# Optimization experiments

Hardware: AMD Instinct MI355X
Metric: run time of the kernel (lower is better)

Reference implementation:

```python
import jax, jax.numpy as jnp
import numpy as np

B, S, H = 1, 2048, 1024
NH, KVH, HD = 16, 4, 64
E, TOPK, F = 8, 2, 2048
EPS = 1e-5
THETA = 10000.0


def setup_inputs() -> dict:
    key = jax.random.key(0)
    ks = jax.random.split(key, 12)
    s = 0.02
    return {
        "hidden_states": jax.random.normal(ks[0], (B, S, H), jnp.float32),
        "position_ids": jnp.arange(S, dtype=jnp.int64).reshape(1, S),
        "ln1_w": jnp.ones((H,), jnp.float32),
        "ln2_w": jnp.ones((H,), jnp.float32),
        "wq": jax.random.normal(ks[1], (NH * HD, H), jnp.float32) * s,
        "wk": jax.random.normal(ks[2], (KVH * HD, H), jnp.float32) * s,
        "wv": jax.random.normal(ks[3], (KVH * HD, H), jnp.float32) * s,
        "wo": jax.random.normal(ks[4], (H, NH * HD), jnp.float32) * s,
        "gate_w": jax.random.normal(ks[5], (E, H), jnp.float32) * s,
        "w1": jax.random.normal(ks[6], (E, F, H), jnp.float32) * s,
        "w2": jax.random.normal(ks[7], (E, H, F), jnp.float32) * s,
        "w3": jax.random.normal(ks[8], (E, F, H), jnp.float32) * s,
    }


def rmsnorm(x, w, eps=EPS):
    xf = x.astype(jnp.float32)
    v = jnp.mean(xf * xf, axis=-1, keepdims=True)
    return (xf * jax.lax.rsqrt(v + eps)).astype(x.dtype) * w


def rotate_half(x):
    x1, x2 = jnp.split(x, 2, axis=-1)
    return jnp.concatenate([-x2, x1], axis=-1)


def attention(x, position_ids, wq, wk, wv, wo):
    q = (x @ wq.T).reshape(B, S, NH, HD).transpose(0, 2, 1, 3)   # [B,NH,S,HD]
    k = (x @ wk.T).reshape(B, S, KVH, HD).transpose(0, 2, 1, 3)  # [B,KVH,S,HD]
    v = (x @ wv.T).reshape(B, S, KVH, HD).transpose(0, 2, 1, 3)
    inv_freq = 1.0 / (THETA ** (jnp.arange(0, HD, 2, dtype=jnp.float32) / HD))
    ang = position_ids.astype(jnp.float32)[:, :, None] * inv_freq  # [B,S,HD/2]
    emb = jnp.concatenate([ang, ang], axis=-1)                     # [B,S,HD]
    cos = jnp.cos(emb)[:, None]                                    # [B,1,S,HD]
    sin = jnp.sin(emb)[:, None]
    q = q * cos + rotate_half(q) * sin
    k = k * cos + rotate_half(k) * sin
    rep = NH // KVH
    k = jnp.repeat(k, rep, axis=1)
    v = jnp.repeat(v, rep, axis=1)
    scores = jnp.einsum("bhqd,bhkd->bhqk", q, k) / np.sqrt(HD).astype(np.float32)
    causal = jnp.tril(jnp.ones((S, S), bool))
    scores = jnp.where(causal, scores, jnp.finfo(scores.dtype).min)
    attn = jax.nn.softmax(scores, axis=-1)
    ctx = jnp.einsum("bhqk,bhkd->bhqd", attn, v)
    ctx = ctx.transpose(0, 2, 1, 3).reshape(B, S, NH * HD)
    return ctx @ wo.T


def moe(x, gate_w, w1, w2, w3):
    xt = x.reshape(-1, H)                                  # [T,H]
    router_logits = xt @ gate_w.T                          # [T,E]
    probs = jax.nn.softmax(router_logits.astype(jnp.float32), axis=-1)
    topw, topi = jax.lax.top_k(probs, TOPK)                # [T,K]
    topw = topw / jnp.sum(topw, axis=-1, keepdims=True)
    topw = topw.astype(x.dtype)
    # combine weights per expert: [T,E]
    cw = jnp.sum(topw[..., None] * jax.nn.one_hot(topi, E, dtype=x.dtype), axis=1)
    h1 = jnp.einsum("th,efh->etf", xt, w1)
    h3 = jnp.einsum("th,efh->etf", xt, w3)
    g = jax.nn.silu(h1) * h3                               # [E,T,F]
    y = jnp.einsum("etf,ehf->eth", g, w2)                  # [E,T,H]
    out = jnp.einsum("eth,te->th", y, cw)
    return out.reshape(B, S, H), router_logits


def reference(hidden_states, position_ids, ln1_w, ln2_w, wq, wk, wv, wo,
              gate_w, w1, w2, w3):
    residual = hidden_states
    h = rmsnorm(hidden_states, ln1_w)
    h = attention(h, position_ids, wq, wk, wv, wo)
    h = residual + h
    residual = h
    h = rmsnorm(h, ln2_w)
    h, router_logits = moe(h, gate_w, w1, w2, w3)
    h = residual + h
    return h, router_logits
```

## Files before the change

### kernel.cpp

```cpp
#include <hip/hip_runtime.h>
#include <hip/hip_bf16.h>
#include <cstdint>

typedef unsigned short u16;
typedef __attribute__((ext_vector_type(8))) short bh8;
typedef __attribute__((ext_vector_type(4))) short sh4;
typedef __attribute__((ext_vector_type(4))) float fx4;

#define NTOK 2048
#define HDIM 1024
#define NE 8
#define FDIM 2048

#define VMCNT(n) asm volatile("s_waitcnt vmcnt(" #n ")" ::: "memory")
#define LGKM0()  asm volatile("s_waitcnt lgkmcnt(0)" ::: "memory")
#define SBAR()   __builtin_amdgcn_s_barrier()
#define SCB()    __builtin_amdgcn_sched_barrier(0)

__device__ __forceinline__ u16 f2bf(float f) {
    __hip_bfloat16 h = __float2bfloat16(f);
    return __builtin_bit_cast(u16, h);
}

__device__ __forceinline__ void gll16(const void* g, void* l) {
    __builtin_amdgcn_global_load_lds(
        (const __attribute__((address_space(1))) void*)g,
        (__attribute__((address_space(3))) void*)l, 16, 0, 0);
}

#define N8_WQ 131072
#define N8_WK 32768
#define N8_WV 32768
#define N8_WO 131072
#define N8_W  2097152
#define B0q 0
#define B1k (B0q + N8_WQ)
#define B2v (B1k + N8_WK)
#define B3o (B2v + N8_WV)
#define B4a (B3o + N8_WO)
#define B5b (B4a + N8_W)
#define B6c (B5b + N8_W)
#define N8TOT (B6c + N8_W)

__global__ __launch_bounds__(256)
void convert_all_k(const float* __restrict__ wq, const float* __restrict__ wk,
                   const float* __restrict__ wv, const float* __restrict__ wo,
                   const float* __restrict__ w1, const float* __restrict__ w2,
                   const float* __restrict__ w3, u16* __restrict__ arena) {
    int i = blockIdx.x * 256 + threadIdx.x;
    const int stride = gridDim.x * 256;
    for (; i < N8TOT; i += stride) {
        const float* src;
        int base;
        if (i < B1k)      { src = wq; base = B0q; }
        else if (i < B2v) { src = wk; base = B1k; }
        else if (i < B3o) { src = wv; base = B2v; }
        else if (i < B4a) { src = wo; base = B3o; }
        else if (i < B5b) { src = w1; base = B4a; }
        else if (i < B6c) { src = w2; base = B5b; }
        else              { src = w3; base = B6c; }
        const size_t li = (size_t)(i - base) * 8;
        const fx4 a = *(const fx4*)&src[li];
        const fx4 b = *(const fx4*)&src[li + 4];
        bh8 o;
        #pragma unroll
        for (int j = 0; j < 4; ++j) {
            o[j]     = (short)f2bf(a[j]);
            o[j + 4] = (short)f2bf(b[j]);
        }
        *(bh8*)&arena[(size_t)i * 8] = o;
    }
}

__global__ __launch_bounds__(256)
void rope_table_k(float* __restrict__ cosT, float* __restrict__ sinT) {
    int idx = blockIdx.x * 256 + threadIdx.x;
    int t = idx >> 5, i = idx & 31;
    float freq = powf(10000.0f, -(float)i * (1.0f / 32.0f));
    float ang = (float)t * freq;
    float s, c;
    sincosf(ang, &s, &c);
    cosT[idx] = c;
    sinT[idx] = s;
}

__global__ __launch_bounds__(256)
void rmsnorm_k(const float* __restrict__ X, const float* __restrict__ W, u16* __restrict__ O) {
    const int t = blockIdx.x;
    const int tid = threadIdx.x;
    const fx4 v = *(const fx4*)&X[(size_t)t * HDIM + tid * 4];
    float ss = v[0]*v[0] + v[1]*v[1] + v[2]*v[2] + v[3]*v[3];
    #pragma unroll
    for (int o = 1; o < 64; o <<= 1) ss += __shfl_xor(ss, o);
    __shared__ float red[4];
    if ((tid & 63) == 0) red[tid >> 6] = ss;
    __syncthreads();
    const float inv = rsqrtf((red[0] + red[1] + red[2] + red[3]) * (1.0f / HDIM) + 1e-5f);
    const fx4 w = *(const fx4*)&W[tid * 4];
    sh4 o4;
    #pragma unroll
    for (int i = 0; i < 4; ++i) o4[i] = (short)f2bf(v[i] * inv * w[i]);
    *(sh4*)&O[(size_t)t * HDIM + tid * 4] = o4;
}

__global__ __launch_bounds__(256)
void rmsnorm2_router_k(const float* __restrict__ X, const float* __restrict__ W,
                       const float* __restrict__ GW, u16* __restrict__ O,
                       float* __restrict__ LOGI) {
    const int t = blockIdx.x;
    const int tid = threadIdx.x;
    const fx4 v = *(const fx4*)&X[(size_t)t * HDIM + tid * 4];
    float ss = v[0]*v[0] + v[1]*v[1] + v[2]*v[2] + v[3]*v[3];
    #pragma unroll
    for (int o = 1; o < 64; o <<= 1) ss += __shfl_xor(ss, o);
    __shared__ float red[4];
    if ((tid & 63) == 0) red[tid >> 6] = ss;
    __syncthreads();
    const float inv = rsqrtf((red[0] + red[1] + red[2] + red[3]) * (1.0f / HDIM) + 1e-5f);
    const fx4 w = *(const fx4*)&W[tid * 4];
    fx4 xn;
    #pragma unroll
    for (int i = 0; i < 4; ++i) xn[i] = v[i] * inv * w[i];
    sh4 o4;
    #pragma unroll
    for (int i = 0; i < 4; ++i) o4[i] = (short)f2bf(xn[i]);
    *(sh4*)&O[(size_t)t * HDIM + tid * 4] = o4;

    float part[NE];
    #pragma unroll
    for (int e = 0; e < NE; ++e) {
        const fx4 g = *(const fx4*)&GW[(size_t)e * HDIM + tid * 4];
        part[e] = g[0]*xn[0] + g[1]*xn[1] + g[2]*xn[2] + g[3]*xn[3];
    }
    #pragma unroll
    for (int e = 0; e < NE; ++e)
        #pragma unroll
        for (int o = 1; o < 64; o <<= 1) part[e] += __shfl_xor(part[e], o);
    __shared__ float red8[4][NE];
    if ((tid & 63) == 0) {
        #pragma unroll
        for (int e = 0; e < NE; ++e) red8[tid >> 6][e] = part[e];
    }
    __syncthreads();
    if (tid < NE)
        LOGI[(size_t)t * NE + tid] = red8[0][tid] + red8[1][tid] + red8[2][tid] + red8[3][tid];
}

__global__ __launch_bounds__(256)
void router_topk_k(const float* __restrict__ LOGI, int* __restrict__ counts,
                   int* __restrict__ tokslot, float* __restrict__ wtb) {
    const int t = blockIdx.x * 256 + threadIdx.x;
    float l[NE];
    #pragma unroll
    for (int e = 0; e < NE; ++e) l[e] = LOGI[(size_t)t * NE + e];
    int i0 = 0;
    #pragma unroll
    for (int e = 1; e < NE; ++e) if (l[e] > l[i0]) i0 = e;
    int i1 = (i0 == 0) ? 1 : 0;
    #pragma unroll
    for (int e = 0; e < NE; ++e) if (e != i0 && l[e] > l[i1]) i1 = e;
    float e1 = __expf(l[i1] - l[i0]);
    float w0 = 1.0f / (1.0f + e1);
    float w1 = 1.0f - w0;
    int p0 = atomicAdd(&counts[i0], 1);
    tokslot[i0 * NTOK + p0] = t * 2;
    wtb[i0 * NTOK + p0] = w0;
    int p1 = atomicAdd(&counts[i1], 1);
    tokslot[i1 * NTOK + p1] = t * 2 + 1;
    wtb[i1 * NTOK + p1] = w1;
}

template<int EPI>
__global__ __launch_bounds__(256)
void gemm_bt(const u16* __restrict__ A, const u16* __restrict__ B,
             u16* __restrict__ Cb, float* __restrict__ Cf,
             const int N, const int K,
             const float* __restrict__ aux0, const float* __restrict__ aux1) {
    __shared__ u16 As[4][64 * 32];
    __shared__ u16 Bs[4][64 * 32];

    const int tid = threadIdx.x;
    const int lane = tid & 63;
    const int wid = tid >> 6;
    const int lrow = lane & 15, lgrp = lane >> 4;
    const int wm = wid * 16;
    const int soff = (lgrp ^ ((lrow >> 1) & 3)) * 8;

    const int m0 = blockIdx.y * 64;
    const int n0 = blockIdx.x * 64;

    const int gseg = ((tid & 3) ^ ((tid >> 3) & 3)) * 8;
    const u16* apg = A + (size_t)(m0 + (tid >> 2)) * K + gseg;
    const u16* bpg = B + (size_t)(n0 + (tid >> 2)) * K + gseg;

    fx4 acc[4];
    #pragma unroll
    for (int i = 0; i < 4; ++i) acc[i] = fx4{0.f, 0.f, 0.f, 0.f};

#define G_STG(BUF, KK) gll16(apg + (KK), &As[BUF][wid * 512]); \
                       gll16(bpg + (KK), &Bs[BUF][wid * 512]);
#define G_CMP(BUF)                                                             \
    {                                                                          \
        const bh8 af = *(const bh8*)&As[BUF][(wm + lrow) * 32 + soff];         \
        _Pragma("unroll")                                                      \
        for (int ni = 0; ni < 4; ++ni) {                                       \
            const bh8 bf = *(const bh8*)&Bs[BUF][(ni * 16 + lrow) * 32 + soff];\
            acc[ni] = __builtin_amdgcn_mfma_f32_16x16x32_bf16(af, bf, acc[ni], 0, 0, 0); \
        }                                                                      \
    }
#define G_PHASE(BUF_ST, KOFF, BUF_CM)                                          \
    { const int kn = (k0 + (KOFF) < K) ? k0 + (KOFF) : 0; G_STG(BUF_ST, kn) }  \
    VMCNT(6); SBAR(); SCB();                                                   \
    G_CMP(BUF_CM)                                                              \
    LGKM0(); SBAR();

    G_STG(0, 0) G_STG(1, 32) G_STG(2, 64)
    for (int k0 = 0; k0 < K; k0 += 128) {
        G_PHASE(3, 96, 0)
        G_PHASE(0, 128, 1)
        G_PHASE(1, 160, 2)
        G_PHASE(2, 192, 3)
    }
    VMCNT(0);
#undef G_STG
#undef G_CMP
#undef G_PHASE

    if (EPI == 4) {
        #pragma unroll
        for (int ni = 0; ni < 4; ++ni) {
            const int c = n0 + ni * 16 + lrow;
            const int r = m0 + wm + lgrp * 4;
            sh4 o4;
            #pragma unroll
            for (int j = 0; j < 4; ++j) o4[j] = (short)f2bf(acc[ni][j]);
            *(sh4*)&Cb[(size_t)c * NTOK + r] = o4;
        }
        return;
    }

    #pragma unroll
    for (int j = 0; j < 4; ++j) {
        const int r = m0 + wm + lgrp * 4 + j;
        if (EPI == 3) {
            #pragma unroll
            for (int ni = 0; ni < 2; ++ni) {
                const int d = ni * 16 + lrow;
                const float cv = aux0[r * 32 + d];
                const float sv = aux1[r * 32 + d];
                const float v0 = acc[ni][j];
                const float v1 = acc[ni + 2][j];
                Cb[(size_t)r * N + n0 + d]      = f2bf(v0 * cv - v1 * sv);
                Cb[(size_t)r * N + n0 + d + 32] = f2bf(v1 * cv + v0 * sv);
            }
        } else {
            #pragma unroll
            for (int ni = 0; ni < 4; ++ni) {
                const int c = n0 + ni * 16 + lrow;
                const float v = acc[ni][j];
                if (EPI == 1) Cf[(size_t)r * N + c] = v + aux0[(size_t)r * N + c];
                if (EPI == 2) Cb[(size_t)r * N + c] = f2bf(v);
            }
        }
    }
}

__global__ __launch_bounds__(256)
void attn_part_k(const u16* __restrict__ Q, const u16* __restrict__ Kg,
                 const u16* __restrict__ VTg, float* __restrict__ pacc,
                 float* __restrict__ pl) {
    const int qt = blockIdx.x;
    const int h = blockIdx.y;
    const int c = blockIdx.z;
    if (c * 8 > qt) return;
    const int t0 = c * 8;
    const int tend = min(qt + 1, t0 + 8);
    const int kvh = h >> 2;

    const int tid = threadIdx.x;
    const int lane = tid & 63;
    const int wid = tid >> 6;
    const int lrow = lane & 15, lgrp = lane >> 4;

    __shared__ u16 Ks[64 * 66];
    __shared__ u16 Vs[64 * 66];
    __shared__ u16 Ps[4][16 * 66];

    const int qbase = qt * 64 + wid * 16;

    bh8 qf[2];
    #pragma unroll
    for (int kf = 0; kf < 2; ++kf)
        qf[kf] = *(const bh8*)&Q[(size_t)(qbase + lrow) * 1024 + h * 64 + kf * 32 + lgrp * 8];

    fx4 acc[4];
    #pragma unroll
    for (int ni = 0; ni < 4; ++ni) acc[ni] = fx4{0.f, 0.f, 0.f, 0.f};
    float lsum[4];
    #pragma unroll
    for (int j = 0; j < 4; ++j) lsum[j] = 0.f;

    const int srow = tid >> 2;
    const int sseg = (tid & 3) * 16;

    size_t gk = (size_t)(t0 * 64 + srow) * 256 + kvh * 64 + sseg;
    size_t gv = (size_t)(kvh * 64 + srow) * NTOK + t0 * 64 + sseg;
    bh8 kva = *(const bh8*)&Kg[gk];
    bh8 kvb = *(const bh8*)&Kg[gk + 8];
    bh8 vva = *(const bh8*)&VTg[gv];
    bh8 vvb = *(const bh8*)&VTg[gv + 8];

    for (int it = t0; it < tend; ++it) {
        const int kv0 = it * 64;
        __syncthreads();
        *(bh8*)&Ks[srow * 66 + sseg]     = kva;
        *(bh8*)&Ks[srow * 66 + sseg + 8] = kvb;
        *(bh8*)&Vs[srow * 66 + sseg]     = vva;
        *(bh8*)&Vs[srow * 66 + sseg + 8] = vvb;
        __syncthreads();

        const int itn = (it + 1 < tend) ? it + 1 : it;
        const size_t gk2 = (size_t)(itn * 64 + srow) * 256 + kvh * 64 + sseg;
        const size_t gv2 = (size_t)(kvh * 64 + srow) * NTOK + itn * 64 + sseg;
        kva = *(const bh8*)&Kg[gk2];
        kvb = *(const bh8*)&Kg[gk2 + 8];
        vva = *(const bh8*)&VTg[gv2];
        vvb = *(const bh8*)&VTg[gv2 + 8];

        fx4 s[4];
        #pragma unroll
        for (int nf = 0; nf < 4; ++nf) s[nf] = fx4{0.f, 0.f, 0.f, 0.f};
        #pragma unroll
        for (int kf = 0; kf < 2; ++kf) {
            #pragma unroll
            for (int nf = 0; nf < 4; ++nf) {
                const bh8 kfr = *(const bh8*)&Ks[(nf * 16 + lrow) * 66 + kf * 32 + lgrp * 8];
                s[nf] = __builtin_amdgcn_mfma_f32_16x16x32_bf16(qf[kf], kfr, s[nf], 0, 0, 0);
            }
        }

        #pragma unroll
        for (int nf = 0; nf < 4; ++nf)
            #pragma unroll
            for (int j = 0; j < 4; ++j) {
                const int qr = qbase + lgrp * 4 + j;
                const int kp = kv0 + nf * 16 + lrow;
                float p = __expf(fmaf(s[nf][j], 0.125f, -24.0f));
                p = (kp > qr) ? 0.f : p;
                s[nf][j] = p;
                lsum[j] += p;
            }

        u16* pw = Ps[wid];
        #pragma unroll
        for (int nf = 0; nf < 4; ++nf)
            #pragma unroll
            for (int j = 0; j < 4; ++j)
                pw[(lgrp * 4 + j) * 66 + nf * 16 + lrow] = f2bf(s[nf][j]);

        #pragma unroll
        for (int kf = 0; kf < 2; ++kf) {
            const bh8 pa = *(const bh8*)&pw[lrow * 66 + kf * 32 + lgrp * 8];
            #pragma unroll
            for (int ni = 0; ni < 4; ++ni) {
                const bh8 vb = *(const bh8*)&Vs[(ni * 16 + lrow) * 66 + kf * 32 + lgrp * 8];
                acc[ni] = __builtin_amdgcn_mfma_f32_16x16x32_bf16(pa, vb, acc[ni], 0, 0, 0);
            }
        }
    }

    #pragma unroll
    for (int j = 0; j < 4; ++j) {
        float l = lsum[j];
        #pragma unroll
        for (int o = 1; o < 16; o <<= 1) l += __shfl_xor(l, o);
        lsum[j] = l;
    }

    #pragma unroll
    for (int j = 0; j < 4; ++j) {
        const int r = qbase + lgrp * 4 + j;
        const size_t base = ((size_t)(h * NTOK + r) * 4 + c) * 64;
        #pragma unroll
        for (int ni = 0; ni < 4; ++ni)
            pacc[base + ni * 16 + lrow] = acc[ni][j];
        if (lrow == 0)
            pl[(size_t)(h * NTOK + r) * 4 + c] = lsum[j];
    }
}

__global__ __launch_bounds__(256)
void attn_combine_k(const float* __restrict__ pacc, const float* __restrict__ pl,
                    u16* __restrict__ O) {
    const int idx = blockIdx.x * 4 + (threadIdx.x >> 6);
    const int d = threadIdx.x & 63;
    const int h = idx >> 11;
    const int qrow = idx & 2047;
    const int nch = (qrow >> 9) + 1;

    float den = 0.f, num = 0.f;
    for (int c = 0; c < nch; ++c) {
        den += pl[(size_t)idx * 4 + c];
        num += pacc[((size_t)idx * 4 + c) * 64 + d];
    }
    O[(size_t)qrow * 1024 + h * 64 + d] = f2bf(num / den);
}

__global__ __launch_bounds__(256)
void moe_up_k(const u16* __restrict__ X, const u16* __restrict__ W1b,
              const u16* __restrict__ W3b, const int* __restrict__ counts,
              const int* __restrict__ tokslot, u16* __restrict__ G) {
    const int e = blockIdx.z;
    const int cnt = counts[e];
    const int m0 = blockIdx.y * 64;
    if (m0 >= cnt) return;
    const int n0 = blockIdx.x * 128;

    __shared__ u16 As[4][64 * 32];
    __shared__ u16 B1s[4][128 * 32];
    __shared__ u16 B3s[4][128 * 32];

    const int tid = threadIdx.x;
    const int lane = tid & 63, wid = tid >> 6;
    const int wm = (wid >> 1) * 32, wn = (wid & 1) * 64;
    const int lrow = lane & 15, lgrp = lane >> 4;
    const int soff = (lgrp ^ ((lrow >> 1) & 3)) * 8;

    const int gseg = ((tid & 3) ^ ((tid >> 3) & 3)) * 8;
    const int arow = m0 + (tid >> 2);
    const int tok = (arow < cnt) ? (tokslot[e * NTOK + arow] >> 1) : 0;
    const u16* apg = X + (size_t)tok * HDIM + gseg;
    const size_t eoff = (size_t)e * FDIM * HDIM;
    const u16* b1pg = W1b + eoff + (size_t)(n0 + (tid >> 2)) * HDIM + gseg;
    const u16* b3pg = W3b + eoff + (size_t)(n0 + (tid >> 2)) * HDIM + gseg;
    const size_t rr = (size_t)64 * HDIM;

    fx4 acc1[2][4], acc3[2][4];
    #pragma unroll
    for (int i = 0; i < 2; ++i)
        #pragma unroll
        for (int j = 0; j < 4; ++j) {
            acc1[i][j] = fx4{0.f, 0.f, 0.f, 0.f};
            acc3[i][j] = fx4{0.f, 0.f, 0.f, 0.f};
        }

#define U_STG(BUF, KK)                                          \
    gll16(apg + (KK), &As[BUF][wid * 512]);                     \
    gll16(b1pg + (KK), &B1s[BUF][wid * 512]);                   \
    gll16(b1pg + rr + (KK), &B1s[BUF][2048 + wid * 512]);       \
    gll16(b3pg + (KK), &B3s[BUF][wid * 512]);                   \
    gll16(b3pg + rr + (KK), &B3s[BUF][2048 + wid * 512]);

#define U_CMP(BUF)                                                                   \
    {                                                                                \
        bh8 af[2], b1f[4], b3f[4];                                                   \
        _Pragma("unroll")                                                            \
        for (int mi = 0; mi < 2; ++mi)                                               \
            af[mi] = *(const bh8*)&As[BUF][(wm + mi * 16 + lrow) * 32 + soff];       \
        _Pragma("unroll")                                                            \
        for (int ni = 0; ni < 4; ++ni) {                                             \
            b1f[ni] = *(const bh8*)&B1s[BUF][(wn + ni * 16 + lrow) * 32 + soff];     \
            b3f[ni] = *(const bh8*)&B3s[BUF][(wn + ni * 16 + lrow) * 32 + soff];     \
        }                                                                            \
        _Pragma("unroll")                                                            \
        for (int mi = 0; mi < 2; ++mi)                                               \
            _Pragma("unroll")                                                        \
            for (int ni = 0; ni < 4; ++ni) {                                         \
                acc1[mi][ni] = __builtin_amdgcn_mfma_f32_16x16x32_bf16(af[mi], b1f[ni], acc1[mi][ni], 0, 0, 0); \
                acc3[mi][ni] = __builtin_amdgcn_mfma_f32_16x16x32_bf16(af[mi], b3f[ni], acc3[mi][ni], 0, 0, 0); \
            }                                                                        \
    }

#define U_PHASE(BUF_ST, KOFF, BUF_CM)                                          \
    { const int kn = (k0 + (KOFF) < HDIM) ? k0 + (KOFF) : 0; U_STG(BUF_ST, kn) } \
    VMCNT(15); SBAR(); SCB();                                                  \
    U_CMP(BUF_CM)                                                              \
    LGKM0(); SBAR();

    U_STG(0, 0) U_STG(1, 32) U_STG(2, 64)
    for (int k0 = 0; k0 < HDIM; k0 += 128) {
        U_PHASE(3, 96, 0)
        U_PHASE(0, 128, 1)
        U_PHASE(1, 160, 2)
        U_PHASE(2, 192, 3)
    }
    VMCNT(0);
#undef U_STG
#undef U_CMP
#undef U_PHASE

    #pragma unroll
    for (int mi = 0; mi < 2; ++mi)
        #pragma unroll
        for (int j = 0; j < 4; ++j) {
            const int r = m0 + wm + mi * 16 + lgrp * 4 + j;
            if (r < cnt) {
                #pragma unroll
                for (int ni = 0; ni < 4; ++ni) {
                    const int c = n0 + wn + ni * 16 + lrow;
                    const float h1 = acc1[mi][ni][j];
                    const float h3 = acc3[mi][ni][j];
                    const float gv = h1 / (1.0f + __expf(-h1)) * h3;
                    G[((size_t)e * NTOK + r) * FDIM + c] = f2bf(gv);
                }
            }
        }
}

__global__ __launch_bounds__(256)
void moe_down_k(const u16* __restrict__ G, const u16* __restrict__ W2b,
                const int* __restrict__ counts, const int* __restrict__ tokslot,
                const float* __restrict__ wtb, float* __restrict__ MO) {
    const int e = blockIdx.z;
    const int cnt = counts[e];
    const int m0 = blockIdx.y * 64;
    if (m0 >= cnt) return;
    const int n0 = blockIdx.x * 64;

    __shared__ u16 As[4][64 * 32];
    __shared__ u16 Bs[4][64 * 32];

    const int tid = threadIdx.x;
    const int lane = tid & 63;
    const int wid = tid >> 6;
    const int lrow = lane & 15, lgrp = lane >> 4;
    const int wm = wid * 16;
    const int soff = (lgrp ^ ((lrow >> 1) & 3)) * 8;

    const int gseg = ((tid & 3) ^ ((tid >> 3) & 3)) * 8;
    const u16* apg = G + ((size_t)e * NTOK + m0 + (tid >> 2)) * FDIM + gseg;
    const u16* bpg = W2b + (size_t)e * HDIM * FDIM + (size_t)(n0 + (tid >> 2)) * FDIM + gseg;

    fx4 acc[4];
    #pragma unroll
    for (int i = 0; i < 4; ++i) acc[i] = fx4{0.f, 0.f, 0.f, 0.f};

#define D_STG(BUF, KK) gll16(apg + (KK), &As[BUF][wid * 512]); \
                       gll16(bpg + (KK), &Bs[BUF][wid * 512]);
#define D_CMP(BUF)                                                             \
    {                                                                          \
        const bh8 af = *(const bh8*)&As[BUF][(wm + lrow) * 32 + soff];         \
        _Pragma("unroll")                                                      \
        for (int ni = 0; ni < 4; ++ni) {                                       \
            const bh8 bf = *(const bh8*)&Bs[BUF][(ni * 16 + lrow) * 32 + soff];\
            acc[ni] = __builtin_amdgcn_mfma_f32_16x16x32_bf16(af, bf, acc[ni], 0, 0, 0); \
        }                                                                      \
    }
#define D_PHASE(BUF_ST, KOFF, BUF_CM)                                          \
    { const int kn = (k0 + (KOFF) < FDIM) ? k0 + (KOFF) : 0; D_STG(BUF_ST, kn) } \
    VMCNT(6); SBAR(); SCB();                                                   \
    D_CMP(BUF_CM)                                                              \
    LGKM0(); SBAR();

    D_STG(0, 0) D_STG(1, 32) D_STG(2, 64)
    for (int k0 = 0; k0 < FDIM; k0 += 128) {
        D_PHASE(3, 96, 0)
        D_PHASE(0, 128, 1)
        D_PHASE(1, 160, 2)
        D_PHASE(2, 192, 3)
    }
    VMCNT(0);
#undef D_STG
#undef D_CMP
#undef D_PHASE

    #pragma unroll
    for (int j = 0; j < 4; ++j) {
        const int r = m0 + wm + lgrp * 4 + j;
        if (r < cnt) {
            const int ts = tokslot[e * NTOK + r];
            const float wgt = wtb[e * NTOK + r];
            const int tt = ts >> 1;
            const int sl = ts & 1;
            #pragma unroll
            for (int ni = 0; ni < 4; ++ni) {
                const int c = n0 + ni * 16 + lrow;
                MO[((size_t)sl * NTOK + tt) * HDIM + c] = acc[ni][j] * wgt;
            }
        }
    }
}

__global__ __launch_bounds__(256)
void final_add_k(const float* __restrict__ A, const float* __restrict__ B0,
                 const float* __restrict__ B1, float* __restrict__ O) {
    const size_t i = ((size_t)blockIdx.x * 256 + threadIdx.x) * 4;
    const fx4 a = *(const fx4*)&A[i];
    const fx4 b = *(const fx4*)&B0[i];
    const fx4 c = *(const fx4*)&B1[i];
    fx4 r;
    #pragma unroll
    for (int k = 0; k < 4; ++k) r[k] = a[k] + b[k] + c[k];
    *(fx4*)&O[i] = r;
}

extern "C" void kernel_launch(void* const* d_in, const int* in_sizes, int n_in,
                              void* d_out, int out_size, void* d_ws, size_t ws_size,
                              hipStream_t stream) {
    const float* x   = (const float*)d_in[0];
    const float* ln1 = (const float*)d_in[2];
    const float* ln2 = (const float*)d_in[3];
    const float* wq  = (const float*)d_in[4];
    const float* wk  = (const float*)d_in[5];
    const float* wv  = (const float*)d_in[6];
    const float* wo  = (const float*)d_in[7];
    const float* gw  = (const float*)d_in[8];
    const float* w1  = (const float*)d_in[9];
    const float* w2  = (const float*)d_in[10];
    const float* w3  = (const float*)d_in[11];

    float* out_h = (float*)d_out;
    float* out_logits = out_h + (size_t)NTOK * HDIM;

    uint8_t* wsb = (uint8_t*)d_ws;
    size_t off = 0;
    auto alloc = [&](size_t bytes) -> void* {
        void* ptr = wsb + off;
        off = (off + bytes + 255) & ~(size_t)255;
        return ptr;
    };
    u16*   xn1    = (u16*)alloc((size_t)NTOK * HDIM * 2);
    u16*   qb     = (u16*)alloc((size_t)NTOK * 1024 * 2);
    u16*   kb     = (u16*)alloc((size_t)NTOK * 256 * 2);
    u16*   vbt    = (u16*)alloc((size_t)256 * NTOK * 2);
    u16*   ctxb   = (u16*)alloc((size_t)NTOK * 1024 * 2);
    float* hattn  = (float*)alloc((size_t)NTOK * HDIM * 4);
    u16*   xn2    = (u16*)alloc((size_t)NTOK * HDIM * 2);
    float* cosT   = (float*)alloc((size_t)NTOK * 32 * 4);
    float* sinT   = (float*)alloc((size_t)NTOK * 32 * 4);
    int*   counts = (int*)alloc(NE * 4);
    int*   tokslot= (int*)alloc((size_t)NE * NTOK * 4);
    float* wtb    = (float*)alloc((size_t)NE * NTOK * 4);
    u16*   gbuf   = (u16*)alloc((size_t)NE * NTOK * FDIM * 2);
    float* moeb   = (float*)alloc((size_t)2 * NTOK * HDIM * 4);
    u16*   arena  = (u16*)alloc((size_t)N8TOT * 8 * 2);
    u16*   wqb    = arena;
    u16*   wkb    = arena + (size_t)B1k * 8;
    u16*   wvb    = arena + (size_t)B2v * 8;
    u16*   wob    = arena + (size_t)B3o * 8;
    u16*   w1b    = arena + (size_t)B4a * 8;
    u16*   w2b    = arena + (size_t)B5b * 8;
    u16*   w3b    = arena + (size_t)B6c * 8;

    float* pacc = (float*)gbuf;
    float* pl   = pacc + (size_t)16 * NTOK * 4 * 64;

    hipMemsetAsync(counts, 0, NE * 4, stream);

    convert_all_k<<<2048, 256, 0, stream>>>(wq, wk, wv, wo, w1, w2, w3, arena);

    rope_table_k<<<256, 256, 0, stream>>>(cosT, sinT);
    rmsnorm_k<<<NTOK, 256, 0, stream>>>(x, ln1, xn1);
    gemm_bt<3><<<dim3(16, 32), 256, 0, stream>>>(xn1, wqb, qb, nullptr, 1024, HDIM, cosT, sinT);
    gemm_bt<3><<<dim3(4, 32), 256, 0, stream>>>(xn1, wkb, kb, nullptr, 256, HDIM, cosT, sinT);
    gemm_bt<4><<<dim3(4, 32), 256, 0, stream>>>(xn1, wvb, vbt, nullptr, 256, HDIM, nullptr, nullptr);
    attn_part_k<<<dim3(32, 16, 4), 256, 0, stream>>>(qb, kb, vbt, pacc, pl);
    attn_combine_k<<<8192, 256, 0, stream>>>(pacc, pl, ctxb);
    gemm_bt<1><<<dim3(16, 32), 256, 0, stream>>>(ctxb, wob, nullptr, hattn, 1024, 1024, x, nullptr);
    rmsnorm2_router_k<<<NTOK, 256, 0, stream>>>(hattn, ln2, gw, xn2, out_logits);
    router_topk_k<<<8, 256, 0, stream>>>(out_logits, counts, tokslot, wtb);
    moe_up_k<<<dim3(16, 32, NE), 256, 0, stream>>>(xn2, w1b, w3b, counts, tokslot, gbuf);
    moe_down_k<<<dim3(16, 32, NE), 256, 0, stream>>>(gbuf, w2b, counts, tokslot, wtb, moeb);
    final_add_k<<<NTOK, 256, 0, stream>>>(hattn, moeb, moeb + (size_t)NTOK * HDIM, out_h);
}
```

Before: 376.3 us.

## Overlap MoE weight conversion with attention by adding conversion blocks to attention grid

Splits the fp32-to-bf16 weight conversion in two. The small QKVO weights are still converted up front, while the large w1/w2/w3 conversion is moved into extra blocks (z==4) of the attention partial kernel. The aim is to hide the memory-bound conversion behind the compute-bound, causally imbalanced attention work, where many blocks exit early. The risk is that the converter blocks compete with attention for bandwidth and CU slots, and that attention becomes the critical path.

```diff
diff --git a/kernel.cpp b/kernel.cpp
--- a/kernel.cpp
+++ b/kernel.cpp
@@ -41,34 +41,36 @@
 #define B5b (B4a + N8_W)
 #define B6c (B5b + N8_W)
 #define N8TOT (B6c + N8_W)
-
-__global__ __launch_bounds__(256)
-void convert_all_k(const float* __restrict__ wq, const float* __restrict__ wk,
-                   const float* __restrict__ wv, const float* __restrict__ wo,
-                   const float* __restrict__ w1, const float* __restrict__ w2,
-                   const float* __restrict__ w3, u16* __restrict__ arena) {
+#define N8QKVO B4a
+#define N8MOE (3 * N8_W)
+
+__device__ __forceinline__ void conv8(const float* __restrict__ src, size_t li,
+                                      u16* __restrict__ dst, size_t di) {
+    const fx4 a = *(const fx4*)&src[li];
+    const fx4 b = *(const fx4*)&src[li + 4];
+    bh8 o;
+    #pragma unroll
+    for (int j = 0; j < 4; ++j) {
+        o[j]     = (short)f2bf(a[j]);
+        o[j + 4] = (short)f2bf(b[j]);
+    }
+    *(bh8*)&dst[di] = o;
+}
+
+__global__ __launch_bounds__(256)
+void convert_qkvo_k(const float* __restrict__ wq, const float* __restrict__ wk,
+                    const float* __restrict__ wv, const float* __restrict__ wo,
+                    u16* __restrict__ arena) {
     int i = blockIdx.x * 256 + threadIdx.x;
     const int stride = gridDim.x * 256;
-    for (; i < N8TOT; i += stride) {
+    for (; i < N8QKVO; i += stride) {
         const float* src;
         int base;
         if (i < B1k)      { src = wq; base = B0q; }
         else if (i < B2v) { src = wk; base = B1k; }
         else if (i < B3o) { src = wv; base = B2v; }
-        else if (i < B4a) { src = wo; base = B3o; }
-        else if (i < B5b) { src = w1; base = B4a; }
-        else if (i < B6c) { src = w2; base = B5b; }
-        else              { src = w3; base = B6c; }
-        const size_t li = (size_t)(i - base) * 8;
-        const fx4 a = *(const fx4*)&src[li];
-        const fx4 b = *(const fx4*)&src[li + 4];
-        bh8 o;
-        #pragma unroll
-        for (int j = 0; j < 4; ++j) {
-            o[j]     = (short)f2bf(a[j]);
-            o[j + 4] = (short)f2bf(b[j]);
-        }
-        *(bh8*)&arena[(size_t)i * 8] = o;
+        else              { src = wo; base = B3o; }
+        conv8(src, (size_t)(i - base) * 8, arena, (size_t)i * 8);
     }
 }
 
@@ -266,9 +268,26 @@
 }
 
 __global__ __launch_bounds__(256)
-void attn_part_k(const u16* __restrict__ Q, const u16* __restrict__ Kg,
+void attn_conv_k(const u16* __restrict__ Q, const u16* __restrict__ Kg,
                  const u16* __restrict__ VTg, float* __restrict__ pacc,
-                 float* __restrict__ pl) {
+                 float* __restrict__ pl,
+                 const float* __restrict__ w1, const float* __restrict__ w2,
+                 const float* __restrict__ w3, u16* __restrict__ arena_moe) {
+    if (blockIdx.z == 4) {
+        const int bid = blockIdx.y * 32 + blockIdx.x;
+        int i = bid * 256 + threadIdx.x;
+        const int stride = 512 * 256;
+        for (; i < N8MOE; i += stride) {
+            const float* src;
+            int base;
+            if (i < N8_W)          { src = w1; base = 0; }
+            else if (i < 2 * N8_W) { src = w2; base = N8_W; }
+            else                   { src = w3; base = 2 * N8_W; }
+            conv8(src, (size_t)(i - base) * 8, arena_moe, (size_t)i * 8);
+        }
+        return;
+    }
+
     const int qt = blockIdx.x;
     const int h = blockIdx.y;
     const int c = blockIdx.z;
@@ -647,14 +666,15 @@
 
     hipMemsetAsync(counts, 0, NE * 4, stream);
 
-    convert_all_k<<<2048, 256, 0, stream>>>(wq, wk, wv, wo, w1, w2, w3, arena);
+    convert_qkvo_k<<<256, 256, 0, stream>>>(wq, wk, wv, wo, arena);
 
     rope_table_k<<<256, 256, 0, stream>>>(cosT, sinT);
     rmsnorm_k<<<NTOK, 256, 0, stream>>>(x, ln1, xn1);
     gemm_bt<3><<<dim3(16, 32), 256, 0, stream>>>(xn1, wqb, qb, nullptr, 1024, HDIM, cosT, sinT);
     gemm_bt<3><<<dim3(4, 32), 256, 0, stream>>>(xn1, wkb, kb, nullptr, 256, HDIM, cosT, sinT);
     gemm_bt<4><<<dim3(4, 32), 256, 0, stream>>>(xn1, wvb, vbt, nullptr, 256, HDIM, nullptr, nullptr);
-    attn_part_k<<<dim3(32, 16, 4), 256, 0, stream>>>(qb, kb, vbt, pacc, pl);
+    attn_conv_k<<<dim3(32, 16, 5), 256, 0, stream>>>(qb, kb, vbt, pacc, pl,
+                                                     w1, w2, w3, arena + (size_t)B4a * 8);
     attn_combine_k<<<8192, 256, 0, stream>>>(pacc, pl, ctxb);
     gemm_bt<1><<<dim3(16, 32), 256, 0, stream>>>(ctxb, wob, nullptr, hattn, 1024, 1024, x, nullptr);
     rmsnorm2_router_k<<<NTOK, 256, 0, stream>>>(hattn, ln2, gw, xn2, out_logits);
```

After: 368.4 us. 2.1% less time.
